# Performance work log

Hardware: AMD Instinct MI355X
Metric: run time of the kernel (lower is better)

The kernel has to match this reference:

```python
import jax, jax.numpy as jnp
import numpy as np

NU, NI, G, D, HD, OD = 8000, 10000, 4096, 64, 64, 64
ALPHA = 0.8      # self vs neighbor mixing in NodeApplyModule
EPS = 1e-8       # cosine-similarity denominator epsilon
NEG_BIG = -1e38  # replacement for all -inf rows


def setup_inputs() -> dict:
    key = jax.random.key(0)
    ks = jax.random.split(key, 24)
    def lin(k, o, i):
        return (jax.random.normal(k, (o, i), jnp.float32) * 0.02)
    def bias(k, o):
        return (jax.random.normal(k, (o,), jnp.float32) * 0.02)
    inp = {}
    inp["H"] = jax.random.randint(ks[0], (NU + NI, G), 0, 2, jnp.int32)
    inp["feats_weight"] = jax.random.normal(ks[1], (NU + NI, D), jnp.float32) * 0.1
    inp["num_groups"] = G
    # user SelfAttention params
    inp["u_Wq"] = lin(ks[2], HD, D); inp["u_bq"] = bias(ks[3], HD)
    inp["u_Wk"] = lin(ks[4], HD, D); inp["u_bk"] = bias(ks[5], HD)
    inp["u_Wv"] = lin(ks[6], HD, D); inp["u_bv"] = bias(ks[7], HD)
    inp["u_Ws"] = lin(ks[8], 1, NU); inp["u_bs"] = bias(ks[9], 1)
    # item SelfAttention params
    inp["i_Wq"] = lin(ks[10], HD, D); inp["i_bq"] = bias(ks[11], HD)
    inp["i_Wk"] = lin(ks[12], HD, D); inp["i_bk"] = bias(ks[13], HD)
    inp["i_Wv"] = lin(ks[14], HD, D); inp["i_bv"] = bias(ks[15], HD)
    inp["i_Ws"] = lin(ks[16], 1, NI); inp["i_bs"] = bias(ks[17], 1)
    # WeightedGCN NodeApplyModule linear: in_feats = 2*HD -> out_feats = OD
    inp["g_W"] = lin(ks[18], OD, 2 * HD); inp["g_b"] = bias(ks[19], OD)
    return inp


def _self_attention(x, mask, num_groups, Wq, bq, Wk, bk, Wv, bv, Ws, bs):
    # x: [N, D] ; mask: [N, G]
    q = x @ Wq.T + bq            # [N, HD]
    k = x @ Wk.T + bk            # [N, HD]
    v = x @ Wv.T + bv            # [N, HD]
    s = (q @ k.T) @ Ws.T + bs    # [N, 1]  (Linear(num_elem,1) over q@k.T)
    scores = jnp.broadcast_to(s.reshape(1, -1), (num_groups, x.shape[0]))  # [G, N]
    maskT = (mask == 0).T        # [G, N]
    scores = jnp.where(maskT, -jnp.inf, scores)
    all_inf = jnp.all(scores == -jnp.inf, axis=1, keepdims=True)
    scores = jnp.where(all_inf, jnp.float32(NEG_BIG), scores)
    w = jax.nn.softmax(scores, axis=1)   # [G, N]
    return w @ v, w                      # [G, HD], [G, N]


def reference(H, feats_weight, num_groups,
              u_Wq, u_bq, u_Wk, u_bk, u_Wv, u_bv, u_Ws, u_bs,
              i_Wq, i_bq, i_Wk, i_bk, i_Wv, i_bv, i_Ws, i_bs,
              g_W, g_b):
    users_feats = feats_weight[:NU]
    items_feats = feats_weight[NU:]
    users_mask = H[:NU]
    items_mask = H[NU:]

    gf_u, w_u = _self_attention(users_feats, users_mask, num_groups,
                                u_Wq, u_bq, u_Wk, u_bk, u_Wv, u_bv, u_Ws, u_bs)
    gf_i, w_i = _self_attention(items_feats, items_mask, num_groups,
                                i_Wq, i_bq, i_Wk, i_bk, i_Wv, i_bv, i_Ws, i_bs)
    # NaN scrubbing (faithful to torch.where(isnan, 0, .))
    gf_i = jnp.where(jnp.isnan(gf_i), 0.0, gf_i)
    w_i = jnp.where(jnp.isnan(w_i), 0.0, w_i)

    group_weights = jnp.concatenate([w_u, w_i], axis=1)   # [G, NU+NI]
    group_feats = jnp.concatenate([gf_u, gf_i], axis=1)   # [G, 2*HD]

    # similarity graph (cosine similarity of group weight rows)
    wp = group_weights @ group_weights.T                  # [G, G]
    norms = jnp.sqrt(jnp.sum(group_weights * group_weights, axis=1))
    l2 = 1.0 / (norms[:, None] * norms[None, :] + EPS)
    A = wp * l2  # edge weight src->dst at A[src, dst]; zero WP entries contribute 0

    # weighted mean aggregation (DGL msg/reduce: sum(w*h)/sum(w) over in-edges)
    msg = A.T @ group_feats                 # [G, 2*HD]: sum_src A[src,dst]*h[src]
    deg = jnp.sum(A, axis=0)[:, None]       # [G, 1]:   sum_src A[src,dst]
    h_neigh = jnp.where(deg > 0, msg / jnp.where(deg > 0, deg, 1.0), 0.0)

    agg = ALPHA * group_feats + (1.0 - ALPHA) * h_neigh
    out = jax.nn.sigmoid(agg @ g_W.T + g_b)               # [G, OD]
    return out
```

## Files before the change

### kernel.cpp

```cpp
#include <hip/hip_runtime.h>
#include <hip/hip_bf16.h>
#include <cstdint>
#include <cstddef>

#define NU   8000
#define NI   10000
#define NTOT 18000
#define G    4096
#define KP2  18176
#define NSL  284
#define NSL128 142
#define KT8  142
#define UT8  63

typedef __attribute__((ext_vector_type(4))) float f32x4;

__device__ __forceinline__ float bfu(unsigned short u){
  return __uint_as_float(((unsigned)u)<<16);
}
__device__ __forceinline__ unsigned short f2b(float f){
  __hip_bfloat16 h = __float2bfloat16(f);
  return __builtin_bit_cast(unsigned short, h);
}
__device__ __forceinline__ unsigned char f2f8(float v){
  int p = __builtin_amdgcn_cvt_pk_fp8_f32(v, 0.f, 0, false);
  return (unsigned char)(p & 0xff);
}
template<int SEL>
__device__ __forceinline__ float f8tof(unsigned int w){
  return __builtin_amdgcn_cvt_f32_fp8((int)w, SEL);
}
__device__ __forceinline__ void async16(void* lds, const void* g){
  __builtin_amdgcn_global_load_lds((const __attribute__((address_space(1))) unsigned int*)g,
                                   (__attribute__((address_space(3))) unsigned int*)lds, 16, 0, 0);
}
__device__ __forceinline__ int slot2n(int s){
  return (s < 8064) ? (s < 8000 ? s : -1) : (s-64 < NTOT ? s-64 : -1);
}

__global__ __launch_bounds__(256) void k_proj(
    const float* __restrict__ feats,
    const float* uWq, const float* ubq, const float* uWk, const float* ubk,
    const float* uWv, const float* ubv, const float* uWs,
    const float* iWq, const float* ibq, const float* iWk, const float* ibk,
    const float* iWv, const float* ibv, const float* iWs,
    float* __restrict__ q, unsigned short* __restrict__ vrow, float* __restrict__ wsk)
{
  __shared__ unsigned short Wt[6*4096];
  __shared__ float bl[6*64];
  __shared__ float wacc[128];
  const float* mats[6]  = {uWq,uWk,uWv,iWq,iWk,iWv};
  const float* bias6[6] = {ubq,ubk,ubv,ibq,ibk,ibv};
  int t = threadIdx.x;
  for (int m=0;m<6;m++)
    for (int e=t; e<4096; e+=256){
      int dd = e>>6, jj = e&63;
      Wt[m*4096 + jj*64 + dd] = f2b(mats[m][e]);
    }
  for (int e=t; e<384; e+=256) bl[e] = bias6[e>>6][e&63];
  if (t<128) wacc[t]=0.f;
  __syncthreads();
  int wave=t>>6, lane=t&63;
  int gw = blockIdx.x*4+wave, nw = gridDim.x*4;
  float accU=0.f, accI=0.f;
  for (int n=gw; n<NTOT; n+=nw){
    int br = (n>=NU);
    const unsigned short* W = Wt + br*3*4096;
    const float* bb = bl + br*192;
    float x = feats[(size_t)n*64+lane];
    float qd=bb[lane], kd=bb[64+lane], vd=bb[128+lane];
    #pragma unroll 16
    for (int j=0;j<64;j++){
      float xj = __shfl(x, j, 64);
      qd += xj * bfu(W[       j*64+lane]);
      kd += xj * bfu(W[4096 + j*64+lane]);
      vd += xj * bfu(W[8192 + j*64+lane]);
    }
    q[(size_t)n*64+lane] = qd;
    vrow[(size_t)n*64+lane] = f2b(vd);
    float wsn = br ? iWs[n-NU] : uWs[n];
    if (br) accI += wsn*kd; else accU += wsn*kd;
  }
  atomicAdd(&wacc[lane], accU);
  atomicAdd(&wacc[64+lane], accI);
  __syncthreads();
  if (t<128) atomicAdd(&wsk[t], wacc[t]);
}

__global__ __launch_bounds__(256) void k_score(const float* __restrict__ q, const float* __restrict__ wsk,
    const float* ubs, const float* ibs, float* __restrict__ rfs, unsigned char* __restrict__ rbs)
{
  __shared__ float wl[128];
  __shared__ float bs2[2];
  int t=threadIdx.x;
  if (t<128) wl[t]=wsk[t];
  if (t==128) bs2[0]=ubs[0];
  if (t==129) bs2[1]=ibs[0];
  __syncthreads();
  int wave=t>>6, lane=t&63;
  #pragma unroll 4
  for (int i=0;i<32;i++){
    int slot = blockIdx.x*128 + i*4 + wave;
    int n = slot2n(slot);
    int br = (slot>=8064);
    float v = 0.f;
    if (n>=0) v = q[(size_t)n*64+lane] * wl[br*64+lane];
    #pragma unroll
    for (int m=32;m>=1;m>>=1) v += __shfl_xor(v, m, 64);
    if (lane==0){
      if (n>=0){
        unsigned char b = f2f8(expf(v + bs2[br]));
        rbs[slot]=b; rfs[slot]=f8tof<0>((unsigned int)b);
      } else {
        rbs[slot]=0; rfs[slot]=0.f;
      }
    }
  }
}

__global__ __launch_bounds__(256) void k_buildW(
    const int* __restrict__ H, const float* __restrict__ rfs, const unsigned char* __restrict__ rbs,
    unsigned char* __restrict__ W8, unsigned char* __restrict__ W8t,
    float* __restrict__ Zu, float* __restrict__ Zi,
    float* __restrict__ S2u, float* __restrict__ S2i)
{
  __shared__ unsigned char Tb[128*136];
  __shared__ float rl[128];
  __shared__ unsigned char rb[128];
  __shared__ float zp[8][128];
  __shared__ float sp[8][128];
  int t = threadIdx.x;
  int s0 = blockIdx.x*128;
  int g0 = blockIdx.y*128;
  int isItem = (s0 >= 8064);
  if (t < 128){
    int n = slot2n(s0+t);
    rl[t] = (n>=0) ? rfs[s0+t] : 0.f;
    rb[t] = (n>=0) ? rbs[s0+t] : (unsigned char)0;
  }
  __syncthreads();
  int rgrp = t>>5;
  int gq   = (t&31)*4;
  int cc   = gq>>4;
  int gi4  = gq&15;
  float za[4]={0.f,0.f,0.f,0.f}, sa[4]={0.f,0.f,0.f,0.f};
  #pragma unroll
  for (int i=0;i<16;i++){
    int row = i*8 + rgrp;
    int n = slot2n(s0+row);
    uchar4 pk; pk.x=0; pk.y=0; pk.z=0; pk.w=0;
    if (n >= 0){
      int4 hv = *(const int4*)(H + (size_t)n*G + g0 + gq);
      unsigned char rbv = rb[row];
      float rq = rl[row];
      if (hv.x){ pk.x=rbv; za[0]+=rq; sa[0]+=rq*rq; }
      if (hv.y){ pk.y=rbv; za[1]+=rq; sa[1]+=rq*rq; }
      if (hv.z){ pk.z=rbv; za[2]+=rq; sa[2]+=rq*rq; }
      if (hv.w){ pk.w=rbv; za[3]+=rq; sa[3]+=rq*rq; }
    }
    int scc = cc ^ ((row>>3)&7);
    *(uchar4*)(Tb + row*136 + (scc<<4) + gi4) = pk;
  }
  #pragma unroll
  for (int e=0;e<4;e++){ zp[rgrp][gq+e]=za[e]; sp[rgrp][gq+e]=sa[e]; }
  __syncthreads();
  #pragma unroll
  for (int p=0;p<4;p++){
    int row = p*32 + (t>>3);
    int c   = t&7;
    int scc = c ^ ((row>>3)&7);
    uint4 v = *(const uint4*)(Tb + row*136 + (scc<<4));
    *(uint4*)(W8t + (size_t)(s0+row)*G + g0 + (c<<4)) = v;
  }
  #pragma unroll
  for (int p=0;p<4;p++){
    int gl = p*32 + (t>>3);
    int sc = (t&7)*16;
    int gcc = gl>>4, gb = gl&15;
    __align__(16) unsigned char buf[16];
    #pragma unroll
    for (int j=0;j<16;j++){
      int row = sc+j;
      int scc = gcc ^ ((row>>3)&7);
      buf[j] = Tb[row*136 + (scc<<4) + gb];
    }
    *(uint4*)(W8 + (size_t)(g0+gl)*KP2 + s0 + sc) = *(uint4*)buf;
  }
  if (t < 128){
    float z=0.f, s2=0.f;
    #pragma unroll
    for (int j=0;j<8;j++){ z += zp[j][t]; s2 += sp[j][t]; }
    if (isItem){ atomicAdd(&Zi[g0+t], z); atomicAdd(&S2i[g0+t], s2); }
    else       { atomicAdd(&Zu[g0+t], z); atomicAdd(&S2u[g0+t], s2); }
  }
}

__global__ __launch_bounds__(256) void k_mid(
    const float* __restrict__ Zu, const float* __restrict__ Zi,
    const float* __restrict__ S2u, const float* __restrict__ S2i,
    float* __restrict__ Cu, float* __restrict__ Ci,
    float* __restrict__ cnu, float* __restrict__ cni, float* __restrict__ ninv,
    unsigned char* __restrict__ cn8u, unsigned char* __restrict__ cn8i,
    unsigned char* __restrict__ W8, unsigned char* __restrict__ W8t,
    const unsigned short* __restrict__ vrow, unsigned char* __restrict__ vt8)
{
  __shared__ unsigned short tile[64][65];
  int b = blockIdx.x;
  int t = threadIdx.x;
  if (b == 0){
    for (int g=t; g<G; g+=256){
      float zu=Zu[g], zi=Zi[g];
      int fu = !(zu>0.f), fi = !(zi>0.f);
      float cu = fu ? (1.f/(float)NU) : 1.f/zu;
      float ci = fi ? (1.f/(float)NI) : 1.f/zi;
      float nu  = fu ? (1.f/(float)NU) : S2u[g]*cu*cu;
      float ni_ = fi ? (1.f/(float)NI) : S2i[g]*ci*ci;
      float nv = rsqrtf(nu+ni_);
      Cu[g]=cu; Ci[g]=ci; ninv[g]=nv; cnu[g]=cu*nv; cni[g]=ci*nv;
      cn8u[g] = f2f8(cu*nv*64.f);
      cn8i[g] = f2f8(ci*nv*64.f);
      if (fu){ for (int k=0;k<NU;k++){ W8[(size_t)g*KP2+k]=0x38; W8t[(size_t)k*G+g]=0x38; } }
      if (fi){ for (int k=0;k<NI;k++){ W8[(size_t)g*KP2+8064+k]=0x38; W8t[(size_t)(8064+k)*G+g]=0x38; } }
    }
    return;
  }
  int s0 = (b-1)*64;
  int tc = t&63, tr = t>>6;
  #pragma unroll
  for (int i=0;i<16;i++){
    int row = tr+i*4;
    int n = slot2n(s0+row);
    tile[row][tc] = (n>=0) ? vrow[(size_t)n*64+tc] : (unsigned short)0;
  }
  __syncthreads();
  int dOff = (s0 >= 8064) ? 64 : 0;
  #pragma unroll
  for (int i=0;i<16;i++){
    int dd = tr+i*4;
    float v = bfu(tile[tc][dd]) * 16.f;
    vt8[(size_t)(dOff+dd)*KP2 + s0+tc] = f2f8(v);
  }
}

template<int MODE>
__global__ __launch_bounds__(256) void k_gemm(
    const unsigned char* __restrict__ A, const unsigned char* __restrict__ B,
    float* __restrict__ Cs, float* __restrict__ degsl,
    const unsigned char* __restrict__ u8,
    const unsigned char* __restrict__ cn8u, const unsigned char* __restrict__ cn8i,
    float* __restrict__ uslice,
    long ldA, long ldB, long ldc)
{
  __shared__ __align__(16) unsigned char As[2][128*128];
  __shared__ __align__(16) unsigned char Bs[2][128*128];
  int t=threadIdx.x, wave=t>>6, lane=t&63;
  int I=blockIdx.x, J=blockIdx.y, z=blockIdx.z;
  int kt0=0, ktn=0;
  if (MODE==0){ kt0 = z*9; ktn = min(9, KT8-kt0); }
  else if (MODE==1){ kt0 = z*8; ktn = 8; }
  else {
    if (z<8){ kt0 = z*8;             ktn = min(8, UT8-kt0); }
    else    { kt0 = UT8 + (z-8)*10;  ktn = min(10, KT8-kt0); }
  }
  f32x4 acc[4][4];
  #pragma unroll
  for (int mi=0;mi<4;mi++)
    #pragma unroll
    for (int ni=0;ni<4;ni++){
      acc[mi][ni][0]=0.f; acc[mi][ni][1]=0.f; acc[mi][ni][2]=0.f; acc[mi][ni][3]=0.f;
    }
  f32x4 accd[4];
  if (MODE==2){
    #pragma unroll
    for (int mi=0;mi<4;mi++){ accd[mi][0]=0.f; accd[mi][1]=0.f; accd[mi][2]=0.f; accd[mi][3]=0.f; }
  }
  f32x4 accu[4];
  if (MODE==1){
    #pragma unroll
    for (int ni=0;ni<4;ni++){ accu[ni][0]=0.f; accu[ni][1]=0.f; accu[ni][2]=0.f; accu[ni][3]=0.f; }
  }
  int l7 = lane&7, q4 = lane>>4, cl15 = lane&15;
  int rowOff = wave*8 + (lane>>3);
  int cchunk = (lane&7) ^ ((lane>>3)&7);
  long aRow0 = (MODE==1) ? ((J>=UT8)?128:0) : (long)I*128;
  const unsigned char* Abase = A + aRow0*ldA + (long)cchunk*16;
  const unsigned char* Bbase = B + (long)J*128*ldB + (long)cchunk*16;
  const unsigned char* cnrow = (MODE==1) ? ((J>=UT8) ? cn8i : cn8u) : nullptr;
  int mrow0 = (wave&1)*64, nrow0 = (wave>>1)*64;

  auto STAGE = [&](int buf, int kt){
    long k0 = (long)kt*128;
    #pragma unroll
    for (int rr=0; rr<4; rr++){
      async16(As[buf] + wave*1024 + rr*4096, Abase + (long)(rr*32 + rowOff)*ldA + k0);
      async16(Bs[buf] + wave*1024 + rr*4096, Bbase + (long)(rr*32 + rowOff)*ldB + k0);
    }
  };

  STAGE(0, kt0);
  __syncthreads();

  for (int kt=kt0; kt<kt0+ktn; ++kt){
    int cur = (kt - kt0) & 1;
    if (kt+1 < kt0+ktn) STAGE(cur^1, kt+1);
    const unsigned char* Ab = As[cur];
    const unsigned char* Bb = Bs[cur];
    #pragma unroll
    for (int kk=0; kk<4; kk++){
      int xoff = (((kk*2 + (q4>>1)) ^ l7) << 4) + ((q4&1)<<3);
      long af[4], bf[4];
      #pragma unroll
      for (int mi=0;mi<4;mi++)
        af[mi] = *(const long*)(Ab + (mrow0 + mi*16 + cl15)*128 + xoff);
      #pragma unroll
      for (int ni=0;ni<4;ni++)
        bf[ni] = *(const long*)(Bb + (nrow0 + ni*16 + cl15)*128 + xoff);
      #pragma unroll
      for (int mi=0;mi<4;mi++)
        #pragma unroll
        for (int ni=0;ni<4;ni++)
          acc[mi][ni] = __builtin_amdgcn_mfma_f32_16x16x32_fp8_fp8(af[mi], bf[ni], acc[mi][ni], 0,0,0);
      if (MODE==2){
        long bu = 0;
        if (cl15==0) bu = *(const long*)(u8 + (size_t)kt*128 + kk*32 + q4*8);
        #pragma unroll
        for (int mi=0;mi<4;mi++)
          accd[mi] = __builtin_amdgcn_mfma_f32_16x16x32_fp8_fp8(af[mi], bu, accd[mi], 0,0,0);
      }
      if (MODE==1){
        long au = 0;
        if (cl15==0) au = *(const long*)(cnrow + (size_t)kt*128 + kk*32 + q4*8);
        #pragma unroll
        for (int ni=0;ni<4;ni++)
          accu[ni] = __builtin_amdgcn_mfma_f32_16x16x32_fp8_fp8(au, bf[ni], accu[ni], 0,0,0);
      }
    }
    __syncthreads();
  }
  int cq = lane>>4, cl = lane&15;
  float* slice = (MODE==1) ? (Cs + (size_t)z*128*KP2) : (Cs + (size_t)z*G*128);
  #pragma unroll
  for (int mi=0;mi<4;mi++)
    #pragma unroll
    for (int ni=0;ni<4;ni++)
      #pragma unroll
      for (int rg=0;rg<4;rg++){
        int gi = (MODE==1 ? 0 : I*128) + mrow0 + mi*16 + cq*4 + rg;
        int hi = J*128 + nrow0 + ni*16 + cl;
        slice[(size_t)gi*ldc + hi] = acc[mi][ni][rg];
      }
  if (MODE==2 && (wave>>1)==0 && cl15==0){
    #pragma unroll
    for (int mi=0;mi<4;mi++)
      #pragma unroll
      for (int rg=0;rg<4;rg++){
        int gi = I*128 + mrow0 + mi*16 + cq*4 + rg;
        degsl[(size_t)z*G + gi] = accd[mi][rg];
      }
  }
  if (MODE==1 && (wave&1)==0 && q4==0){
    #pragma unroll
    for (int ni=0;ni<4;ni++){
      int si = J*128 + nrow0 + ni*16 + cl15;
      uslice[(size_t)z*KP2 + si] = accu[ni][0];
    }
  }
}

__global__ __launch_bounds__(256) void k_gfpost(const float* __restrict__ gfsl,
    const float* __restrict__ Cu, const float* __restrict__ Ci, const float* __restrict__ ninv,
    float* __restrict__ gf, unsigned char* __restrict__ gfsT2_8)
{
  __shared__ float tile[64][65];
  int g0 = blockIdx.x*64, d0 = blockIdx.y*64;
  int tc=threadIdx.x&63, tr=threadIdx.x>>6;
  const float* Cd = blockIdx.y ? Ci : Cu;
  #pragma unroll
  for (int i=0;i<16;i++){
    int rr=tr+i*4;
    size_t off = (size_t)(g0+rr)*128 + d0+tc;
    float s = 0.f;
    #pragma unroll
    for (int zz=0;zz<16;zz++) s += gfsl[(size_t)zz*G*128 + off];
    float gfv = s * Cd[g0+rr] * 0.0625f;
    gf[off] = gfv;
    tile[rr][tc] = gfv * ninv[g0+rr];
  }
  __syncthreads();
  #pragma unroll
  for (int i=0;i<16;i++){
    int dd=tr+i*4;
    float v = tile[tc][dd] * 64.f;
    int g = g0+tc;
    gfsT2_8[(size_t)(d0+dd)*G + g]     = f2f8(v*Cu[g]);
    gfsT2_8[(size_t)(128+d0+dd)*G + g] = f2f8(v*Ci[g]);
  }
}

__global__ __launch_bounds__(256) void k_red1(const float* __restrict__ tmpsl,
    unsigned char* __restrict__ tmpT8, const float* __restrict__ uslice, unsigned char* __restrict__ u8){
  int b = blockIdx.x, t = threadIdx.x;
  if (b >= 2272){
    int idx2 = (b-2272)*256 + t;
    if (idx2 < KP2/4){
      size_t off = (size_t)idx2*4;
      f32x4 s = *(const f32x4*)(uslice + off);
      #pragma unroll
      for (int z=1;z<4;z++){
        f32x4 v = *(const f32x4*)(uslice + (size_t)z*KP2 + off);
        s[0]+=v[0]; s[1]+=v[1]; s[2]+=v[2]; s[3]+=v[3];
      }
      uchar4 pk;
      pk.x = f2f8(s[0]*0.015625f);
      pk.y = f2f8(s[1]*0.015625f);
      pk.z = f2f8(s[2]*0.015625f);
      pk.w = f2f8(s[3]*0.015625f);
      *(uchar4*)(u8 + off) = pk;
    }
    return;
  }
  int idx = b*256 + t;
  int d = idx / 4544;
  int n = (idx - d*4544)*4;
  size_t off = (size_t)d*KP2 + n;
  f32x4 s = *(const f32x4*)(tmpsl + off);
  #pragma unroll
  for (int z=1;z<4;z++){
    f32x4 v = *(const f32x4*)(tmpsl + (size_t)z*128*KP2 + off);
    s[0]+=v[0]; s[1]+=v[1]; s[2]+=v[2]; s[3]+=v[3];
  }
  uchar4 pk;
  pk.x = f2f8(s[0]); pk.y = f2f8(s[1]); pk.z = f2f8(s[2]); pk.w = f2f8(s[3]);
  *(uchar4*)(tmpT8 + off) = pk;
}

__global__ __launch_bounds__(256) void k_red2(const float* __restrict__ msgsl,
    const float* __restrict__ cnu, const float* __restrict__ cni, float* __restrict__ msg){
  int idx = blockIdx.x*256 + threadIdx.x;
  int gi = idx>>5;
  int hc = (idx&31)*4;
  size_t off = (size_t)gi*128 + hc;
  f32x4 su = {0.f,0.f,0.f,0.f}, si = {0.f,0.f,0.f,0.f};
  #pragma unroll
  for (int z=0;z<8;z++){
    f32x4 v = *(const f32x4*)(msgsl + (size_t)z*G*128 + off);
    su[0]+=v[0]; su[1]+=v[1]; su[2]+=v[2]; su[3]+=v[3];
  }
  #pragma unroll
  for (int z=8;z<16;z++){
    f32x4 v = *(const f32x4*)(msgsl + (size_t)z*G*128 + off);
    si[0]+=v[0]; si[1]+=v[1]; si[2]+=v[2]; si[3]+=v[3];
  }
  float a = cnu[gi]*0.015625f, b = cni[gi]*0.015625f;
  f32x4 r = {su[0]*a+si[0]*b, su[1]*a+si[1]*b, su[2]*a+si[2]*b, su[3]*a+si[3]*b};
  *(f32x4*)(msg + off) = r;
}

__global__ __launch_bounds__(256) void k_final(const float* __restrict__ gf, const float* __restrict__ msg,
    const float* __restrict__ degsl, const float* __restrict__ cnu, const float* __restrict__ cni,
    const float* __restrict__ gW, const float* __restrict__ gb, float* __restrict__ out)
{
  __shared__ float Wl[64*129];
  __shared__ float aggL[4][128];
  __shared__ float gbL[64];
  __shared__ float degL[4];
  int t=threadIdx.x;
  for (int e=t; e<8192; e+=256){ int o=e>>7, dd=e&127; Wl[o*129+dd] = gW[e]; }
  if (t<64) gbL[t] = gb[t];
  int g0 = blockIdx.x*4;
  if (t<4){
    int g = g0+t;
    float su=0.f, si=0.f;
    #pragma unroll
    for (int z=0;z<8;z++) su += degsl[(size_t)z*G + g];
    #pragma unroll
    for (int z=8;z<16;z++) si += degsl[(size_t)z*G + g];
    degL[t] = cnu[g]*su + cni[g]*si;
  }
  __syncthreads();
  for (int e=t; e<512; e+=256){
    int gl=e>>7, dd=e&127; int g=g0+gl;
    float dv = degL[gl];
    float hn = dv>0.f ? msg[(size_t)g*128+dd]/dv : 0.f;
    aggL[gl][dd] = 0.8f*gf[(size_t)g*128+dd] + 0.2f*hn;
  }
  __syncthreads();
  int gl = t>>6, o = t&63;
  float s = gbL[o];
  #pragma unroll
  for (int dd=0; dd<128; dd++) s += aggL[gl][dd]*Wl[o*129+dd];
  out[(size_t)(g0+gl)*64 + o] = 1.f/(1.f+expf(-s));
}

extern "C" void kernel_launch(void* const* d_in, const int* in_sizes, int n_in,
                              void* d_out, int out_size, void* d_ws, size_t ws_size,
                              hipStream_t stream)
{
  (void)in_sizes; (void)n_in; (void)out_size; (void)ws_size;
  const int* H = (const int*)d_in[0];
  const float* feats = (const float*)d_in[1];
  const float* uWq=(const float*)d_in[3];
  const float* ubq=(const float*)d_in[4];
  const float* uWk=(const float*)d_in[5];
  const float* ubk=(const float*)d_in[6];
  const float* uWv=(const float*)d_in[7];
  const float* ubv=(const float*)d_in[8];
  const float* uWs=(const float*)d_in[9];
  const float* ubs=(const float*)d_in[10];
  const float* iWq=(const float*)d_in[11];
  const float* ibq=(const float*)d_in[12];
  const float* iWk=(const float*)d_in[13];
  const float* ibk=(const float*)d_in[14];
  const float* iWv=(const float*)d_in[15];
  const float* ibv=(const float*)d_in[16];
  const float* iWs=(const float*)d_in[17];
  const float* ibs=(const float*)d_in[18];
  const float* gW =(const float*)d_in[19];
  const float* gb =(const float*)d_in[20];
  float* out = (float*)d_out;

  char* p = (char*)d_ws;
  auto alloc=[&](size_t b)->void*{ void* r=(void*)p; p += (b+255)&~(size_t)255; return r; };
  char* zbase = p;
  float* wsk  = (float*)alloc(128*4);
  float* Zu   = (float*)alloc(G*4);
  float* Zi   = (float*)alloc(G*4);
  float* S2u  = (float*)alloc(G*4);
  float* S2i  = (float*)alloc(G*4);
  unsigned char* vt8 = (unsigned char*)alloc((size_t)128*KP2);
  size_t zlen = (size_t)(p - zbase);
  unsigned char* W8    = (unsigned char*)alloc((size_t)G*KP2);
  unsigned char* W8t   = (unsigned char*)alloc((size_t)KP2*G);
  unsigned char* tmpT8 = (unsigned char*)alloc((size_t)128*KP2);
  unsigned char* gfsT2_8=(unsigned char*)alloc((size_t)256*G);
  float* slb  = (float*)alloc((size_t)4*128*KP2*4);
  float* uslice=(float*)alloc((size_t)4*KP2*4);
  float* degsl= (float*)alloc((size_t)16*G*4);
  float* gf   = (float*)alloc((size_t)G*128*4);
  float* msg  = (float*)alloc((size_t)G*128*4);
  float* q    = (float*)alloc((size_t)NTOT*64*4);
  unsigned short* vrow=(unsigned short*)alloc((size_t)NTOT*64*2);
  float* rfs  = (float*)alloc((size_t)KP2*4);
  unsigned char* rbs = (unsigned char*)alloc((size_t)KP2);
  float* Cu   = (float*)alloc(G*4);
  float* Ci   = (float*)alloc(G*4);
  float* cnu  = (float*)alloc(G*4);
  float* cni  = (float*)alloc(G*4);
  float* ninv = (float*)alloc(G*4);
  unsigned char* cn8u = (unsigned char*)alloc(G);
  unsigned char* cn8i = (unsigned char*)alloc(G);
  unsigned char* u8 = (unsigned char*)alloc((size_t)KP2);

  (void)hipMemsetAsync(zbase, 0, zlen, stream);

  k_proj<<<256,256,0,stream>>>(feats, uWq,ubq,uWk,ubk,uWv,ubv,uWs,
                               iWq,ibq,iWk,ibk,iWv,ibv,iWs, q, vrow, wsk);
  k_score<<<KP2/128,256,0,stream>>>(q, wsk, ubs, ibs, rfs, rbs);
  k_buildW<<<dim3(NSL128,32),256,0,stream>>>(H, rfs, rbs, W8, W8t, Zu, Zi, S2u, S2i);
  k_mid<<<NSL+1,256,0,stream>>>(Zu,Zi,S2u,S2i,Cu,Ci,cnu,cni,ninv,cn8u,cn8i,W8,W8t,vrow,vt8);
  k_gemm<0><<<dim3(32,1,16),256,0,stream>>>(W8, vt8, slb, nullptr, nullptr, nullptr, nullptr, nullptr,
                                           (long)KP2, (long)KP2, 128);
  k_gfpost<<<dim3(64,2),256,0,stream>>>(slb, Cu, Ci, ninv, gf, gfsT2_8);
  k_gemm<1><<<dim3(1,KT8,4),256,0,stream>>>(gfsT2_8, W8t, slb, nullptr, nullptr, cn8u, cn8i, uslice,
                                            (long)G, (long)G, (long)KP2);
  k_red1<<<2272+18,256,0,stream>>>(slb, tmpT8, uslice, u8);
  k_gemm<2><<<dim3(32,1,16),256,0,stream>>>(W8, tmpT8, slb, degsl, u8, nullptr, nullptr, nullptr,
                                           (long)KP2, (long)KP2, 128);
  k_red2<<<512,256,0,stream>>>(slb, cnu, cni, msg);
  k_final<<<G/4,256,0,stream>>>(gf, msg, degsl, cnu, cni, gW, gb, out);
}
```

Before: 700.9 us.

## Store membership matrices as bitmasks and expand to fp8 operands inside GEMMs

Replaces the fp8 weight matrices W8/W8t (G x KP2 bytes each) with 1-bit membership bitmaps, plus a per-slot fp8 score vector. The GEMM kernels stage the bitmaps and expand them in registers to fp8 MFMA operands by masking with the replicated score byte. This cuts write and read traffic of the big weight matrices about eightfold. It also folds the k_red2 slice reduction into k_final. It adds ALU work for expansion and atomicOr-based fallback filling in k_mid.

```diff
diff --git a/kernel.cpp b/kernel.cpp
--- a/kernel.cpp
+++ b/kernel.cpp
@@ -12,6 +12,8 @@
 #define NSL128 142
 #define KT8  142
 #define UT8  63
+#define KP2B 2272
+#define GB8  512
 
 typedef __attribute__((ext_vector_type(4))) float f32x4;
 
@@ -36,6 +38,9 @@
 }
 __device__ __forceinline__ int slot2n(int s){
   return (s < 8064) ? (s < 8000 ? s : -1) : (s-64 < NTOT ? s-64 : -1);
+}
+__device__ __forceinline__ unsigned int mask4(unsigned int n){
+  return ((n*0x00204081u)&0x01010101u)*0xFFu;
 }
 
 __global__ __launch_bounds__(256) void k_proj(
@@ -118,78 +123,71 @@
   }
 }
 
-__global__ __launch_bounds__(256) void k_buildW(
-    const int* __restrict__ H, const float* __restrict__ rfs, const unsigned char* __restrict__ rbs,
-    unsigned char* __restrict__ W8, unsigned char* __restrict__ W8t,
+__global__ __launch_bounds__(256) void k_buildB(
+    const int* __restrict__ H, const float* __restrict__ rfs,
+    unsigned char* __restrict__ Wb, unsigned char* __restrict__ Wbt,
     float* __restrict__ Zu, float* __restrict__ Zi,
     float* __restrict__ S2u, float* __restrict__ S2i)
 {
-  __shared__ unsigned char Tb[128*136];
+  __shared__ __align__(16) unsigned char Bt[128][16];
   __shared__ float rl[128];
-  __shared__ unsigned char rb[128];
-  __shared__ float zp[8][128];
-  __shared__ float sp[8][128];
+  __shared__ float zp[16][128];
+  __shared__ float sp[16][128];
   int t = threadIdx.x;
-  int s0 = blockIdx.x*128;
-  int g0 = blockIdx.y*128;
+  int s0 = blockIdx.x*128, g0 = blockIdx.y*128;
   int isItem = (s0 >= 8064);
-  if (t < 128){
-    int n = slot2n(s0+t);
-    rl[t] = (n>=0) ? rfs[s0+t] : 0.f;
-    rb[t] = (n>=0) ? rbs[s0+t] : (unsigned char)0;
-  }
-  __syncthreads();
-  int rgrp = t>>5;
-  int gq   = (t&31)*4;
-  int cc   = gq>>4;
-  int gi4  = gq&15;
-  float za[4]={0.f,0.f,0.f,0.f}, sa[4]={0.f,0.f,0.f,0.f};
-  #pragma unroll
-  for (int i=0;i<16;i++){
-    int row = i*8 + rgrp;
+  if (t<128){ int n = slot2n(s0+t); rl[t] = (n>=0)? rfs[s0+t] : 0.f; }
+  __syncthreads();
+  int gb = t&15, rbase = t>>4;
+  float za[8]={0.f,0.f,0.f,0.f,0.f,0.f,0.f,0.f};
+  float sa[8]={0.f,0.f,0.f,0.f,0.f,0.f,0.f,0.f};
+  #pragma unroll
+  for (int i=0;i<8;i++){
+    int row = rbase + i*16;
     int n = slot2n(s0+row);
-    uchar4 pk; pk.x=0; pk.y=0; pk.z=0; pk.w=0;
-    if (n >= 0){
-      int4 hv = *(const int4*)(H + (size_t)n*G + g0 + gq);
-      unsigned char rbv = rb[row];
-      float rq = rl[row];
-      if (hv.x){ pk.x=rbv; za[0]+=rq; sa[0]+=rq*rq; }
-      if (hv.y){ pk.y=rbv; za[1]+=rq; sa[1]+=rq*rq; }
-      if (hv.z){ pk.z=rbv; za[2]+=rq; sa[2]+=rq*rq; }
-      if (hv.w){ pk.w=rbv; za[3]+=rq; sa[3]+=rq*rq; }
-    }
-    int scc = cc ^ ((row>>3)&7);
-    *(uchar4*)(Tb + row*136 + (scc<<4) + gi4) = pk;
-  }
-  #pragma unroll
-  for (int e=0;e<4;e++){ zp[rgrp][gq+e]=za[e]; sp[rgrp][gq+e]=sa[e]; }
-  __syncthreads();
-  #pragma unroll
-  for (int p=0;p<4;p++){
-    int row = p*32 + (t>>3);
-    int c   = t&7;
-    int scc = c ^ ((row>>3)&7);
-    uint4 v = *(const uint4*)(Tb + row*136 + (scc<<4));
-    *(uint4*)(W8t + (size_t)(s0+row)*G + g0 + (c<<4)) = v;
-  }
-  #pragma unroll
-  for (int p=0;p<4;p++){
-    int gl = p*32 + (t>>3);
-    int sc = (t&7)*16;
-    int gcc = gl>>4, gb = gl&15;
-    __align__(16) unsigned char buf[16];
-    #pragma unroll
-    for (int j=0;j<16;j++){
-      int row = sc+j;
-      int scc = gcc ^ ((row>>3)&7);
-      buf[j] = Tb[row*136 + (scc<<4) + gb];
-    }
-    *(uint4*)(W8 + (size_t)(g0+gl)*KP2 + s0 + sc) = *(uint4*)buf;
-  }
-  if (t < 128){
+    unsigned int b8 = 0;
+    if (n>=0){
+      const int* hp = H + (size_t)n*G + g0 + gb*8;
+      int4 h0 = *(const int4*)hp;
+      int4 h1 = *(const int4*)(hp+4);
+      float rq = rl[row], rq2 = rq*rq;
+      if (h0.x){ b8|=1u;    za[0]+=rq; sa[0]+=rq2; }
+      if (h0.y){ b8|=2u;    za[1]+=rq; sa[1]+=rq2; }
+      if (h0.z){ b8|=4u;    za[2]+=rq; sa[2]+=rq2; }
+      if (h0.w){ b8|=8u;    za[3]+=rq; sa[3]+=rq2; }
+      if (h1.x){ b8|=16u;   za[4]+=rq; sa[4]+=rq2; }
+      if (h1.y){ b8|=32u;   za[5]+=rq; sa[5]+=rq2; }
+      if (h1.z){ b8|=64u;   za[6]+=rq; sa[6]+=rq2; }
+      if (h1.w){ b8|=128u;  za[7]+=rq; sa[7]+=rq2; }
+    }
+    Bt[row][gb] = (unsigned char)b8;
+  }
+  #pragma unroll
+  for (int j=0;j<8;j++){ zp[rbase][gb*8+j]=za[j]; sp[rbase][gb*8+j]=sa[j]; }
+  __syncthreads();
+  {
+    int row = t>>1, half = t&1;
+    *(unsigned long long*)(Wbt + (size_t)(s0+row)*GB8 + (g0>>3) + half*8) =
+        *(const unsigned long long*)(&Bt[row][half*8]);
+  }
+  {
+    int g = t>>1, sh = t&1;
+    int gB = g>>3, gs = g&7;
+    unsigned long long ob = 0;
+    #pragma unroll
+    for (int sb=0; sb<8; sb++){
+      int base = (sh*8+sb)*8;
+      unsigned int x = 0;
+      #pragma unroll
+      for (int j=0;j<8;j++) x |= (((unsigned int)(Bt[base+j][gB]) >> gs)&1u) << j;
+      ob |= (unsigned long long)x << (sb*8);
+    }
+    *(unsigned long long*)(Wb + (size_t)(g0+g)*KP2B + (s0>>3) + sh*8) = ob;
+  }
+  if (t<128){
     float z=0.f, s2=0.f;
     #pragma unroll
-    for (int j=0;j<8;j++){ z += zp[j][t]; s2 += sp[j][t]; }
+    for (int j=0;j<16;j++){ z += zp[j][t]; s2 += sp[j][t]; }
     if (isItem){ atomicAdd(&Zi[g0+t], z); atomicAdd(&S2i[g0+t], s2); }
     else       { atomicAdd(&Zu[g0+t], z); atomicAdd(&S2u[g0+t], s2); }
   }
@@ -201,7 +199,7 @@
     float* __restrict__ Cu, float* __restrict__ Ci,
     float* __restrict__ cnu, float* __restrict__ cni, float* __restrict__ ninv,
     unsigned char* __restrict__ cn8u, unsigned char* __restrict__ cn8i,
-    unsigned char* __restrict__ W8, unsigned char* __restrict__ W8t,
+    unsigned char* __restrict__ Wb, unsigned char* __restrict__ Wbt,
     const unsigned short* __restrict__ vrow, unsigned char* __restrict__ vt8)
 {
   __shared__ unsigned short tile[64][65];
@@ -219,8 +217,16 @@
       Cu[g]=cu; Ci[g]=ci; ninv[g]=nv; cnu[g]=cu*nv; cni[g]=ci*nv;
       cn8u[g] = f2f8(cu*nv*64.f);
       cn8i[g] = f2f8(ci*nv*64.f);
-      if (fu){ for (int k=0;k<NU;k++){ W8[(size_t)g*KP2+k]=0x38; W8t[(size_t)k*G+g]=0x38; } }
-      if (fi){ for (int k=0;k<NI;k++){ W8[(size_t)g*KP2+8064+k]=0x38; W8t[(size_t)(8064+k)*G+g]=0x38; } }
+      if (fu){
+        for (int k=0;k<1000;k++) Wb[(size_t)g*KP2B+k]=0xFF;
+        for (int k=0;k<NU;k++)
+          atomicOr((unsigned*)Wbt + (((size_t)k*GB8 + (g>>3))>>2), 1u<<((g&7) + 8*((g>>3)&3)));
+      }
+      if (fi){
+        for (int k=1008;k<2258;k++) Wb[(size_t)g*KP2B+k]=0xFF;
+        for (int k=8064;k<18064;k++)
+          atomicOr((unsigned*)Wbt + (((size_t)k*GB8 + (g>>3))>>2), 1u<<((g&7) + 8*((g>>3)&3)));
+      }
     }
     return;
   }
@@ -248,11 +254,13 @@
     float* __restrict__ Cs, float* __restrict__ degsl,
     const unsigned char* __restrict__ u8,
     const unsigned char* __restrict__ cn8u, const unsigned char* __restrict__ cn8i,
-    float* __restrict__ uslice,
-    long ldA, long ldB, long ldc)
-{
-  __shared__ __align__(16) unsigned char As[2][128*128];
-  __shared__ __align__(16) unsigned char Bs[2][128*128];
+    float* __restrict__ uslice, const unsigned char* __restrict__ rbsg,
+    long ldF, long ldc)
+{
+  __shared__ __align__(16) unsigned char BufF[2][16384];
+  __shared__ __align__(16) unsigned char BufB[2][2048];
+  __shared__ __align__(16) unsigned char AuxR[2][1024];
+  __shared__ unsigned int RowDw[128];
   int t=threadIdx.x, wave=t>>6, lane=t&63;
   int I=blockIdx.x, J=blockIdx.y, z=blockIdx.z;
   int kt0=0, ktn=0;
@@ -282,19 +290,25 @@
   int l7 = lane&7, q4 = lane>>4, cl15 = lane&15;
   int rowOff = wave*8 + (lane>>3);
   int cchunk = (lane&7) ^ ((lane>>3)&7);
-  long aRow0 = (MODE==1) ? ((J>=UT8)?128:0) : (long)I*128;
-  const unsigned char* Abase = A + aRow0*ldA + (long)cchunk*16;
-  const unsigned char* Bbase = B + (long)J*128*ldB + (long)cchunk*16;
+  long aRow0 = (MODE==1) ? ((J>=UT8)?128:0) : 0;
+  const unsigned char* Fbase;
+  const unsigned char* Bitbase;
+  if (MODE==1){ Fbase = A + aRow0*ldF + (long)cchunk*16; Bitbase = B + (long)J*128*GB8; }
+  else        { Fbase = B + (long)cchunk*16;             Bitbase = A + (long)I*128*KP2B; }
   const unsigned char* cnrow = (MODE==1) ? ((J>=UT8) ? cn8i : cn8u) : nullptr;
   int mrow0 = (wave&1)*64, nrow0 = (wave>>1)*64;
 
+  if (MODE==1 && t<128) RowDw[t] = 0x01010101u * (unsigned int)rbsg[(size_t)J*128 + t];
+
   auto STAGE = [&](int buf, int kt){
     long k0 = (long)kt*128;
     #pragma unroll
-    for (int rr=0; rr<4; rr++){
-      async16(As[buf] + wave*1024 + rr*4096, Abase + (long)(rr*32 + rowOff)*ldA + k0);
-      async16(Bs[buf] + wave*1024 + rr*4096, Bbase + (long)(rr*32 + rowOff)*ldB + k0);
-    }
+    for (int rr=0; rr<4; rr++)
+      async16(BufF[buf] + wave*1024 + rr*4096, Fbase + (long)(rr*32 + rowOff)*ldF + k0);
+    if (wave<2)
+      async16(BufB[buf] + wave*1024, Bitbase + (long)(wave*64+lane)*(MODE==1?GB8:KP2B) + (long)kt*16);
+    if (MODE!=1 && wave==2)
+      async16(AuxR[buf], rbsg + (long)kt*128 + (long)(lane&7)*16);
   };
 
   STAGE(0, kt0);
@@ -303,18 +317,38 @@
   for (int kt=kt0; kt<kt0+ktn; ++kt){
     int cur = (kt - kt0) & 1;
     if (kt+1 < kt0+ktn) STAGE(cur^1, kt+1);
-    const unsigned char* Ab = As[cur];
-    const unsigned char* Bb = Bs[cur];
+    const unsigned char* Fb = BufF[cur];
+    const unsigned char* Bb = BufB[cur];
     #pragma unroll
     for (int kk=0; kk<4; kk++){
       int xoff = (((kk*2 + (q4>>1)) ^ l7) << 4) + ((q4&1)<<3);
+      int kb = kk*4 + q4;
       long af[4], bf[4];
-      #pragma unroll
-      for (int mi=0;mi<4;mi++)
-        af[mi] = *(const long*)(Ab + (mrow0 + mi*16 + cl15)*128 + xoff);
-      #pragma unroll
-      for (int ni=0;ni<4;ni++)
-        bf[ni] = *(const long*)(Bb + (nrow0 + ni*16 + cl15)*128 + xoff);
+      if (MODE==1){
+        #pragma unroll
+        for (int mi=0;mi<4;mi++)
+          af[mi] = *(const long*)(Fb + (mrow0 + mi*16 + cl15)*128 + xoff);
+        #pragma unroll
+        for (int ni=0;ni<4;ni++){
+          int row = nrow0 + ni*16 + cl15;
+          unsigned int bb = Bb[row*16 + kb];
+          unsigned int sp = RowDw[row];
+          unsigned int lo = mask4(bb&15u)&sp, hi = mask4(bb>>4)&sp;
+          bf[ni] = (long)(((unsigned long long)hi<<32)|(unsigned long long)lo);
+        }
+      } else {
+        unsigned long long rdw = *(const unsigned long long*)(AuxR[cur] + kb*8);
+        unsigned int rlo = (unsigned int)rdw, rhi = (unsigned int)(rdw>>32);
+        #pragma unroll
+        for (int mi=0;mi<4;mi++){
+          unsigned int bb = Bb[(mrow0 + mi*16 + cl15)*16 + kb];
+          unsigned int lo = mask4(bb&15u)&rlo, hi = mask4(bb>>4)&rhi;
+          af[mi] = (long)(((unsigned long long)hi<<32)|(unsigned long long)lo);
+        }
+        #pragma unroll
+        for (int ni=0;ni<4;ni++)
+          bf[ni] = *(const long*)(Fb + (nrow0 + ni*16 + cl15)*128 + xoff);
+      }
       #pragma unroll
       for (int mi=0;mi<4;mi++)
         #pragma unroll
@@ -434,29 +468,7 @@
   *(uchar4*)(tmpT8 + off) = pk;
 }
 
-__global__ __launch_bounds__(256) void k_red2(const float* __restrict__ msgsl,
-    const float* __restrict__ cnu, const float* __restrict__ cni, float* __restrict__ msg){
-  int idx = blockIdx.x*256 + threadIdx.x;
-  int gi = idx>>5;
-  int hc = (idx&31)*4;
-  size_t off = (size_t)gi*128 + hc;
-  f32x4 su = {0.f,0.f,0.f,0.f}, si = {0.f,0.f,0.f,0.f};
-  #pragma unroll
-  for (int z=0;z<8;z++){
-    f32x4 v = *(const f32x4*)(msgsl + (size_t)z*G*128 + off);
-    su[0]+=v[0]; su[1]+=v[1]; su[2]+=v[2]; su[3]+=v[3];
-  }
-  #pragma unroll
-  for (int z=8;z<16;z++){
-    f32x4 v = *(const f32x4*)(msgsl + (size_t)z*G*128 + off);
-    si[0]+=v[0]; si[1]+=v[1]; si[2]+=v[2]; si[3]+=v[3];
-  }
-  float a = cnu[gi]*0.015625f, b = cni[gi]*0.015625f;
-  f32x4 r = {su[0]*a+si[0]*b, su[1]*a+si[1]*b, su[2]*a+si[2]*b, su[3]*a+si[3]*b};
-  *(f32x4*)(msg + off) = r;
-}
-
-__global__ __launch_bounds__(256) void k_final(const float* __restrict__ gf, const float* __restrict__ msg,
+__global__ __launch_bounds__(256) void k_final(const float* __restrict__ gf, const float* __restrict__ msgsl,
     const float* __restrict__ degsl, const float* __restrict__ cnu, const float* __restrict__ cni,
     const float* __restrict__ gW, const float* __restrict__ gb, float* __restrict__ out)
 {
@@ -480,9 +492,16 @@
   __syncthreads();
   for (int e=t; e<512; e+=256){
     int gl=e>>7, dd=e&127; int g=g0+gl;
+    size_t off = (size_t)g*128 + dd;
+    float su=0.f, si=0.f;
+    #pragma unroll
+    for (int z=0;z<8;z++)  su += msgsl[(size_t)z*G*128 + off];
+    #pragma unroll
+    for (int z=8;z<16;z++) si += msgsl[(size_t)z*G*128 + off];
+    float mv = (cnu[g]*su + cni[g]*si)*0.015625f;
     float dv = degL[gl];
-    float hn = dv>0.f ? msg[(size_t)g*128+dd]/dv : 0.f;
-    aggL[gl][dd] = 0.8f*gf[(size_t)g*128+dd] + 0.2f*hn;
+    float hn = dv>0.f ? mv/dv : 0.f;
+    aggL[gl][dd] = 0.8f*gf[off] + 0.2f*hn;
   }
   __syncthreads();
   int gl = t>>6, o = t&63;
@@ -529,15 +548,14 @@
   float* S2i  = (float*)alloc(G*4);
   unsigned char* vt8 = (unsigned char*)alloc((size_t)128*KP2);
   size_t zlen = (size_t)(p - zbase);
-  unsigned char* W8    = (unsigned char*)alloc((size_t)G*KP2);
-  unsigned char* W8t   = (unsigned char*)alloc((size_t)KP2*G);
+  unsigned char* Wb    = (unsigned char*)alloc((size_t)G*KP2B);
+  unsigned char* Wbt   = (unsigned char*)alloc((size_t)KP2*GB8);
   unsigned char* tmpT8 = (unsigned char*)alloc((size_t)128*KP2);
   unsigned char* gfsT2_8=(unsigned char*)alloc((size_t)256*G);
   float* slb  = (float*)alloc((size_t)4*128*KP2*4);
   float* uslice=(float*)alloc((size_t)4*KP2*4);
   float* degsl= (float*)alloc((size_t)16*G*4);
   float* gf   = (float*)alloc((size_t)G*128*4);
-  float* msg  = (float*)alloc((size_t)G*128*4);
   float* q    = (float*)alloc((size_t)NTOT*64*4);
   unsigned short* vrow=(unsigned short*)alloc((size_t)NTOT*64*2);
   float* rfs  = (float*)alloc((size_t)KP2*4);
@@ -556,16 +574,15 @@
   k_proj<<<256,256,0,stream>>>(feats, uWq,ubq,uWk,ubk,uWv,ubv,uWs,
                                iWq,ibq,iWk,ibk,iWv,ibv,iWs, q, vrow, wsk);
   k_score<<<KP2/128,256,0,stream>>>(q, wsk, ubs, ibs, rfs, rbs);
-  k_buildW<<<dim3(NSL128,32),256,0,stream>>>(H, rfs, rbs, W8, W8t, Zu, Zi, S2u, S2i);
-  k_mid<<<NSL+1,256,0,stream>>>(Zu,Zi,S2u,S2i,Cu,Ci,cnu,cni,ninv,cn8u,cn8i,W8,W8t,vrow,vt8);
-  k_gemm<0><<<dim3(32,1,16),256,0,stream>>>(W8, vt8, slb, nullptr, nullptr, nullptr, nullptr, nullptr,
-                                           (long)KP2, (long)KP2, 128);
+  k_buildB<<<dim3(NSL128,32),256,0,stream>>>(H, rfs, Wb, Wbt, Zu, Zi, S2u, S2i);
+  k_mid<<<NSL+1,256,0,stream>>>(Zu,Zi,S2u,S2i,Cu,Ci,cnu,cni,ninv,cn8u,cn8i,Wb,Wbt,vrow,vt8);
+  k_gemm<0><<<dim3(32,1,16),256,0,stream>>>(Wb, vt8, slb, nullptr, nullptr, nullptr, nullptr, nullptr,
+                                            rbs, (long)KP2, 128);
   k_gfpost<<<dim3(64,2),256,0,stream>>>(slb, Cu, Ci, ninv, gf, gfsT2_8);
-  k_gemm<1><<<dim3(1,KT8,4),256,0,stream>>>(gfsT2_8, W8t, slb, nullptr, nullptr, cn8u, cn8i, uslice,
-                                            (long)G, (long)G, (long)KP2);
+  k_gemm<1><<<dim3(1,KT8,4),256,0,stream>>>(gfsT2_8, Wbt, slb, nullptr, nullptr, cn8u, cn8i, uslice,
+                                            rbs, (long)G, (long)KP2);
   k_red1<<<2272+18,256,0,stream>>>(slb, tmpT8, uslice, u8);
-  k_gemm<2><<<dim3(32,1,16),256,0,stream>>>(W8, tmpT8, slb, degsl, u8, nullptr, nullptr, nullptr,
-                                           (long)KP2, (long)KP2, 128);
-  k_red2<<<512,256,0,stream>>>(slb, cnu, cni, msg);
-  k_final<<<G/4,256,0,stream>>>(gf, msg, degsl, cnu, cni, gW, gb, out);
-}
+  k_gemm<2><<<dim3(32,1,16),256,0,stream>>>(Wb, tmpT8, slb, degsl, u8, nullptr, nullptr, nullptr,
+                                            rbs, (long)KP2, 128);
+  k_final<<<G/4,256,0,stream>>>(gf, slb, degsl, cnu, cni, gW, gb, out);
+}
```

Measured after the change: 682.7 us. -2.6%, faster.
